# Performance work log

Measured on AMD Instinct MI355X. Metric: run time of the kernel, lower is better.

## Reference

```python
import jax, jax.numpy as jnp
import numpy as np

N = 100_000
E = 1_600_000
F_IN = 128
HEADS = 8
OUT_H = 8   # per-head channels, concat -> 64
N_CLS = 40
K_HOPS = 10  # truncation order of heat-kernel Taylor series
NEG_SLOPE = 0.2
T_INIT = 5.0


def setup_inputs() -> dict:
    key = jax.random.key(0)
    ks = jax.random.split(key, 10)
    x = jax.random.normal(ks[0], (N, F_IN), jnp.float32)
    edge_index = jax.random.randint(ks[1], (2, E), 0, N, jnp.int32)
    t = jnp.full((F_IN,), T_INIT, jnp.float32)  # per-channel learnable diffusion time
    W1 = jax.random.normal(ks[2], (F_IN, HEADS * OUT_H), jnp.float32) / np.sqrt(F_IN).astype(np.float32)
    a_src1 = jax.random.normal(ks[3], (HEADS, OUT_H), jnp.float32) * 0.1
    a_dst1 = jax.random.normal(ks[4], (HEADS, OUT_H), jnp.float32) * 0.1
    b1 = jnp.zeros((HEADS * OUT_H,), jnp.float32)
    W2 = jax.random.normal(ks[5], (HEADS * OUT_H, N_CLS), jnp.float32) / np.sqrt(HEADS * OUT_H).astype(np.float32)
    a_src2 = jax.random.normal(ks[6], (1, N_CLS), jnp.float32) * 0.1
    a_dst2 = jax.random.normal(ks[7], (1, N_CLS), jnp.float32) * 0.1
    b2 = jnp.zeros((N_CLS,), jnp.float32)
    return {"x": x, "edge_index": edge_index, "t": t, "W1": W1, "a_src1": a_src1,
            "a_dst1": a_dst1, "b1": b1, "W2": W2, "a_src2": a_src2, "a_dst2": a_dst2, "b2": b2}


def _add_self_loops(edge_index, n):
    loop = jnp.arange(n, dtype=edge_index.dtype)
    return jnp.concatenate([edge_index, jnp.stack([loop, loop])], axis=1)


def _diffusion(x, src, dst, t, n):
    # heat kernel: exp(-t) * sum_k t^k/k! * A_hat^k x, per-channel t
    deg = jax.ops.segment_sum(jnp.ones_like(src, jnp.float32), dst, num_segments=n)
    dinv = jnp.where(deg > 0, jax.lax.rsqrt(jnp.maximum(deg, 1.0)), 0.0)
    norm = dinv[src] * dinv[dst]  # [E+N]

    def prop(h):
        return jax.ops.segment_sum(norm[:, None] * h[src], dst, num_segments=n)

    coef0 = jnp.exp(-t)  # [F]

    def step(carry, k):
        h, coef, acc = carry
        h = prop(h)
        coef = coef * t / k
        return (h, coef, acc + coef * h), None

    (_, _, out), _ = jax.lax.scan(step, (x, coef0, coef0 * x),
                                  jnp.arange(1, K_HOPS + 1, dtype=jnp.float32))
    return out


def _gat_layer(x, src, dst, W, a_s, a_d, b, heads, out_ch, concat, n):
    h = (x @ W).reshape(n, heads, out_ch)                  # [N,H,C]
    al_s = jnp.einsum('nhc,hc->nh', h, a_s)                # src attn logits
    al_d = jnp.einsum('nhc,hc->nh', h, a_d)
    e = jax.nn.leaky_relu(al_s[src] + al_d[dst], NEG_SLOPE)  # [E+N, H]
    emax = jax.ops.segment_max(e, dst, num_segments=n)       # stable softmax per target node
    ex = jnp.exp(e - emax[dst])
    denom = jax.ops.segment_sum(ex, dst, num_segments=n)
    alpha = ex / jnp.maximum(denom[dst], 1e-16)               # [E+N, H]
    out = jax.ops.segment_sum(alpha[:, :, None] * h[src], dst, num_segments=n)  # [N,H,C]
    out = out.reshape(n, heads * out_ch) if concat else out.mean(axis=1)
    return out + b


def reference(x, edge_index, t, W1, a_src1, a_dst1, b1, W2, a_src2, a_dst2, b2):
    n = x.shape[0]
    ei = _add_self_loops(edge_index, n)
    src, dst = ei[0], ei[1]
    h = _diffusion(x, src, dst, t, n)
    h = _gat_layer(h, src, dst, W1, a_src1, a_dst1, b1, HEADS, OUT_H, True, n)
    h = jax.nn.elu(h)
    h = _gat_layer(h, src, dst, W2, a_src2, a_dst2, b2, 1, N_CLS, False, n)
    return jax.nn.log_softmax(h, axis=1)
```

## Files before the change

kernel.cpp:

```cpp
#include <hip/hip_runtime.h>
#include <hip/hip_bf16.h>


static __device__ __forceinline__ unsigned pack_bf16x2(float a, float b) {
    __hip_bfloat162 p(__float2bfloat16(a), __float2bfloat16(b));
    return *reinterpret_cast<unsigned*>(&p);
}

__global__ void init_node_kernel(int* deg, int n) {
    int i = blockIdx.x * 256 + threadIdx.x;
    if (i < n) deg[i] = 1;
}

__global__ void edge_deg_kernel(const int* __restrict__ dst, int* deg, int* epos, int E) {
    int e = blockIdx.x * 256 + threadIdx.x;
    if (e < E) epos[e] = atomicAdd(&deg[dst[e]], 1);
}

__global__ void alloc_kernel(const int* __restrict__ deg, float* dinv,
                             int* row_off, int* gcount, int n) {
    int i = blockIdx.x * 256 + threadIdx.x;
    if (i >= n) return;
    int dg = deg[i];
    dinv[i] = rsqrtf((float)dg);
    row_off[i] = atomicAdd(gcount, dg);
}

__global__ void scatter_kernel(const int* __restrict__ ei, const int* __restrict__ row_off,
                               const int* __restrict__ epos, const float* __restrict__ dinv,
                               int2* __restrict__ csr_pair, int E, int n) {
    int e = blockIdx.x * 256 + threadIdx.x;
    if (e < E) {
        int s = ei[e], d = ei[E + e];
        csr_pair[row_off[d] + epos[e]] = make_int2(s, __float_as_int(dinv[s] * dinv[d]));
    } else if (e < E + n) {
        int i = e - E;
        float di = dinv[i];
        csr_pair[row_off[i]] = make_int2(i, __float_as_int(di * di));
    }
}

__global__ void coef_kernel(const float* __restrict__ t, float* coefs) {
    int c = threadIdx.x;
    float tc = t[c];
    float v = expf(-tc);
    coefs[c] = v;
    for (int k = 1; k <= 10; ++k) { v *= tc / (float)k; coefs[k * 128 + c] = v; }
}

__global__ void init_diff_a_kernel(const float4* __restrict__ x4, uint2* __restrict__ h0,
                                   int total4) {
    int i = blockIdx.x * 256 + threadIdx.x;
    if (i >= total4) return;
    float4 xv = x4[i];
    h0[i] = make_uint2(pack_bf16x2(xv.x, xv.y), pack_bf16x2(xv.z, xv.w));
}

__global__ void init_diff_b_kernel(const float4* __restrict__ x4, const float* __restrict__ coefs,
                                   uint2* __restrict__ h0, float4* __restrict__ acc4, int total4) {
    int i = blockIdx.x * 256 + threadIdx.x;
    if (i >= total4) return;
    float4 xv = x4[i];
    h0[i] = make_uint2(pack_bf16x2(xv.x, xv.y), pack_bf16x2(xv.z, xv.w));
    const float4 c = *(const float4*)&coefs[(i & 31) * 4];
    acc4[i] = make_float4(c.x * xv.x, c.y * xv.y, c.z * xv.z, c.w * xv.w);
}

static __device__ __forceinline__ float2 gather_row(
    const int* __restrict__ row_off, const int* __restrict__ deg,
    const int2* __restrict__ csr_pair, const unsigned* __restrict__ h,
    int wid, int lane) {
    int off = row_off[wid];
    int cnt = deg[wid];
    float2 a0 = {0.f, 0.f}, a1 = {0.f, 0.f}, a2 = {0.f, 0.f}, a3 = {0.f, 0.f};
    for (int base = 0; base < cnt; base += 64) {
        int nb = min(64, cnt - base);
        int2 p = {0, 0};
        if (lane < nb) p = csr_pair[off + base + lane];
        int tt = 0;
        for (; tt + 7 < nb; tt += 8) {
            int s0 = __builtin_amdgcn_readlane(p.x, tt);
            int s1 = __builtin_amdgcn_readlane(p.x, tt + 1);
            int s2 = __builtin_amdgcn_readlane(p.x, tt + 2);
            int s3 = __builtin_amdgcn_readlane(p.x, tt + 3);
            int s4 = __builtin_amdgcn_readlane(p.x, tt + 4);
            int s5 = __builtin_amdgcn_readlane(p.x, tt + 5);
            int s6 = __builtin_amdgcn_readlane(p.x, tt + 6);
            int s7 = __builtin_amdgcn_readlane(p.x, tt + 7);
            float w0 = __int_as_float(__builtin_amdgcn_readlane(p.y, tt));
            float w1 = __int_as_float(__builtin_amdgcn_readlane(p.y, tt + 1));
            float w2 = __int_as_float(__builtin_amdgcn_readlane(p.y, tt + 2));
            float w3 = __int_as_float(__builtin_amdgcn_readlane(p.y, tt + 3));
            float w4 = __int_as_float(__builtin_amdgcn_readlane(p.y, tt + 4));
            float w5 = __int_as_float(__builtin_amdgcn_readlane(p.y, tt + 5));
            float w6 = __int_as_float(__builtin_amdgcn_readlane(p.y, tt + 6));
            float w7 = __int_as_float(__builtin_amdgcn_readlane(p.y, tt + 7));
            unsigned u0 = h[(size_t)s0 * 64 + lane];
            unsigned u1 = h[(size_t)s1 * 64 + lane];
            unsigned u2 = h[(size_t)s2 * 64 + lane];
            unsigned u3 = h[(size_t)s3 * 64 + lane];
            unsigned u4 = h[(size_t)s4 * 64 + lane];
            unsigned u5 = h[(size_t)s5 * 64 + lane];
            unsigned u6 = h[(size_t)s6 * 64 + lane];
            unsigned u7 = h[(size_t)s7 * 64 + lane];
            a0.x = fmaf(w0, __uint_as_float(u0 << 16), a0.x);
            a0.y = fmaf(w0, __uint_as_float(u0 & 0xffff0000u), a0.y);
            a1.x = fmaf(w1, __uint_as_float(u1 << 16), a1.x);
            a1.y = fmaf(w1, __uint_as_float(u1 & 0xffff0000u), a1.y);
            a2.x = fmaf(w2, __uint_as_float(u2 << 16), a2.x);
            a2.y = fmaf(w2, __uint_as_float(u2 & 0xffff0000u), a2.y);
            a3.x = fmaf(w3, __uint_as_float(u3 << 16), a3.x);
            a3.y = fmaf(w3, __uint_as_float(u3 & 0xffff0000u), a3.y);
            a0.x = fmaf(w4, __uint_as_float(u4 << 16), a0.x);
            a0.y = fmaf(w4, __uint_as_float(u4 & 0xffff0000u), a0.y);
            a1.x = fmaf(w5, __uint_as_float(u5 << 16), a1.x);
            a1.y = fmaf(w5, __uint_as_float(u5 & 0xffff0000u), a1.y);
            a2.x = fmaf(w6, __uint_as_float(u6 << 16), a2.x);
            a2.y = fmaf(w6, __uint_as_float(u6 & 0xffff0000u), a2.y);
            a3.x = fmaf(w7, __uint_as_float(u7 << 16), a3.x);
            a3.y = fmaf(w7, __uint_as_float(u7 & 0xffff0000u), a3.y);
        }
        for (; tt < nb; ++tt) {
            int s = __builtin_amdgcn_readlane(p.x, tt);
            float w = __int_as_float(__builtin_amdgcn_readlane(p.y, tt));
            unsigned u = h[(size_t)s * 64 + lane];
            a0.x = fmaf(w, __uint_as_float(u << 16), a0.x);
            a0.y = fmaf(w, __uint_as_float(u & 0xffff0000u), a0.y);
        }
    }
    float2 s;
    s.x = (a0.x + a1.x) + (a2.x + a3.x);
    s.y = (a0.y + a1.y) + (a2.y + a3.y);
    return s;
}

__global__ void hop_a_kernel(const int* __restrict__ row_off, const int* __restrict__ deg,
                             const int2* __restrict__ csr_pair,
                             const unsigned* __restrict__ h_prev, unsigned* __restrict__ h_out,
                             int n) {
    int wid = (blockIdx.x << 2) + (threadIdx.x >> 6);
    int lane = threadIdx.x & 63;
    if (wid >= n) return;
    float2 s = gather_row(row_off, deg, csr_pair, h_prev, wid, lane);
    h_out[(size_t)wid * 64 + lane] = pack_bf16x2(s.x, s.y);
}

__global__ void hop_b_kernel(const int* __restrict__ row_off, const int* __restrict__ deg,
                             const int2* __restrict__ csr_pair,
                             const unsigned* __restrict__ h_prev, unsigned* __restrict__ h_out,
                             float2* __restrict__ acc2, const float2* __restrict__ coefk2,
                             int n, int write_h) {
    int wid = (blockIdx.x << 2) + (threadIdx.x >> 6);
    int lane = threadIdx.x & 63;
    if (wid >= n) return;
    float2 s = gather_row(row_off, deg, csr_pair, h_prev, wid, lane);
    size_t o = (size_t)wid * 64 + lane;
    if (write_h) h_out[o] = pack_bf16x2(s.x, s.y);
    float2 c = coefk2[lane];
    float2 av = acc2[o];
    av.x = fmaf(c.x, s.x, av.x);
    av.y = fmaf(c.y, s.y, av.y);
    acc2[o] = av;
}

__global__ void combine_kernel(const float2* __restrict__ x2, const float* __restrict__ coefs,
                               const unsigned* __restrict__ hseq, size_t stride,
                               float2* __restrict__ acc2, int total) {
    int i = blockIdx.x * 256 + threadIdx.x;
    if (i >= total) return;
    int c2 = i & 63;
    const float2* coefs2 = (const float2*)coefs;
    float2 c0 = coefs2[c2];
    float2 xv = x2[i];
    float2 a = make_float2(c0.x * xv.x, c0.y * xv.y);
#pragma unroll
    for (int k = 1; k <= 10; ++k) {
        float2 ck = coefs2[(size_t)k * 64 + c2];
        unsigned u = hseq[(size_t)k * stride + i];
        a.x = fmaf(ck.x, __uint_as_float(u << 16), a.x);
        a.y = fmaf(ck.y, __uint_as_float(u & 0xffff0000u), a.y);
    }
    acc2[i] = a;
}

__global__ __launch_bounds__(256) void gemm1_kernel(
    const float* __restrict__ acc, const float* __restrict__ W1,
    const float* __restrict__ a_s, const float* __restrict__ a_d,
    unsigned* __restrict__ h1b, float* __restrict__ als, float* __restrict__ ald, int n) {
    __shared__ float Wl[128 * 64];
    __shared__ float Al[4][16 * 128];
    for (int i = threadIdx.x; i < 128 * 64; i += 256) Wl[i] = W1[i];
    int w = threadIdx.x >> 6;
    int lane = threadIdx.x & 63;
    int node0 = (blockIdx.x * 4 + w) * 16;
    const float4* accv4 = (const float4*)acc;
    float4* Av4 = (float4*)Al[w];
#pragma unroll
    for (int i = 0; i < 8; ++i) {
        int f4 = i * 64 + lane;
        int g4 = node0 * 32 + f4;
        float4 v = (g4 < n * 32) ? accv4[g4] : make_float4(0.f, 0.f, 0.f, 0.f);
        Av4[f4] = v;
    }
    __syncthreads();
    float sums[16];
#pragma unroll
    for (int nd = 0; nd < 16; ++nd) sums[nd] = 0.f;
#pragma unroll 1
    for (int kc = 0; kc < 16; ++kc) {
        float wr[8];
#pragma unroll
        for (int i = 0; i < 8; ++i) wr[i] = Wl[(kc * 8 + i) * 64 + lane];
#pragma unroll
        for (int nd = 0; nd < 16; ++nd) {
            float4 a = *(const float4*)&Al[w][nd * 128 + kc * 8];
            float4 b = *(const float4*)&Al[w][nd * 128 + kc * 8 + 4];
            float s = sums[nd];
            s = fmaf(wr[0], a.x, s); s = fmaf(wr[1], a.y, s);
            s = fmaf(wr[2], a.z, s); s = fmaf(wr[3], a.w, s);
            s = fmaf(wr[4], b.x, s); s = fmaf(wr[5], b.y, s);
            s = fmaf(wr[6], b.z, s); s = fmaf(wr[7], b.w, s);
            sums[nd] = s;
        }
    }
    float asv = a_s[lane], adv = a_d[lane];
#pragma unroll
    for (int nd = 0; nd < 16; ++nd) {
        int node = node0 + nd;
        if (node >= n) break;
        float sum = sums[nd];
        float partner = __shfl_xor(sum, 1);
        if ((lane & 1) == 0) h1b[(size_t)node * 32 + (lane >> 1)] = pack_bf16x2(sum, partner);
        float vs = sum * asv;
        float vd = sum * adv;
        vs += __shfl_xor(vs, 1); vs += __shfl_xor(vs, 2); vs += __shfl_xor(vs, 4);
        vd += __shfl_xor(vd, 1); vd += __shfl_xor(vd, 2); vd += __shfl_xor(vd, 4);
        if ((lane & 7) == 0) {
            als[(size_t)node * 8 + (lane >> 3)] = vs;
            ald[(size_t)node * 8 + (lane >> 3)] = vd;
        }
    }
}

__global__ void agg1_kernel(const int* __restrict__ row_off, const int* __restrict__ deg,
                            const int2* __restrict__ csr_pair,
                            const unsigned* __restrict__ h1b, const float* __restrict__ als,
                            const float* __restrict__ ald, const float* __restrict__ b1,
                            float2* __restrict__ helu2, int n) {
    int wid = (blockIdx.x << 2) + (threadIdx.x >> 6);
    int lane = threadIdx.x & 63;
    if (wid >= n) return;
    int half = lane >> 5;
    int l = lane & 31;
    int head = l >> 2;
    int off = row_off[wid];
    int cnt = deg[wid];
    float aldv = ald[(size_t)wid * 8 + head];
    float dA = 0.f, dB = 0.f;
    float2 aA = {0.f, 0.f}, aB = {0.f, 0.f};
    for (int base = 0; base < cnt; base += 64) {
        int nb = min(64, cnt - base);
        int srcv = 0;
        if (lane < nb) srcv = csr_pair[off + base + lane].x;
        int j = 0;
        for (; j + 3 < nb; j += 4) {
            int sA0 = __builtin_amdgcn_readlane(srcv, j);
            int sA1 = __builtin_amdgcn_readlane(srcv, j + 1);
            int sB0 = __builtin_amdgcn_readlane(srcv, j + 2);
            int sB1 = __builtin_amdgcn_readlane(srcv, j + 3);
            int sA = half ? sA1 : sA0;
            int sB = half ? sB1 : sB0;
            float eA = als[(size_t)sA * 8 + head] + aldv;
            float eB = als[(size_t)sB * 8 + head] + aldv;
            eA = eA > 0.f ? eA : 0.2f * eA;
            eB = eB > 0.f ? eB : 0.2f * eB;
            float pA = __expf(eA);
            float pB = __expf(eB);
            unsigned uA = h1b[(size_t)sA * 32 + l];
            unsigned uB = h1b[(size_t)sB * 32 + l];
            dA += pA; dB += pB;
            aA.x = fmaf(pA, __uint_as_float(uA << 16), aA.x);
            aA.y = fmaf(pA, __uint_as_float(uA & 0xffff0000u), aA.y);
            aB.x = fmaf(pB, __uint_as_float(uB << 16), aB.x);
            aB.y = fmaf(pB, __uint_as_float(uB & 0xffff0000u), aB.y);
        }
        for (; j < nb; j += 2) {
            int s0 = __builtin_amdgcn_readlane(srcv, j);
            int s1 = (j + 1 < nb) ? __builtin_amdgcn_readlane(srcv, j + 1) : -1;
            int s = half ? s1 : s0;
            bool valid = s >= 0;
            int ss = valid ? s : 0;
            float e = als[(size_t)ss * 8 + head] + aldv;
            e = e > 0.f ? e : 0.2f * e;
            float p = valid ? __expf(e) : 0.f;
            unsigned u = h1b[(size_t)ss * 32 + l];
            dA += p;
            aA.x = fmaf(p, __uint_as_float(u << 16), aA.x);
            aA.y = fmaf(p, __uint_as_float(u & 0xffff0000u), aA.y);
        }
    }
    float d = dA + dB;
    float2 accv = make_float2(aA.x + aB.x, aA.y + aB.y);
    d += __shfl_xor(d, 32);
    accv.x += __shfl_xor(accv.x, 32);
    accv.y += __shfl_xor(accv.y, 32);
    if (half == 0) {
        float inv = 1.f / d;
        float ox = fmaf(accv.x, inv, b1[2 * l]);
        float oy = fmaf(accv.y, inv, b1[2 * l + 1]);
        ox = ox > 0.f ? ox : expm1f(ox);
        oy = oy > 0.f ? oy : expm1f(oy);
        helu2[(size_t)wid * 32 + l] = make_float2(ox, oy);
    }
}

__global__ __launch_bounds__(256) void gemm2_kernel(
    const float* __restrict__ helu, const float* __restrict__ W2,
    const float* __restrict__ a_s, const float* __restrict__ a_d,
    unsigned* __restrict__ h2b, float* __restrict__ als, float* __restrict__ ald, int n) {
    __shared__ float Wl[64 * 40];
    __shared__ float Al[4][16 * 64];
    for (int i = threadIdx.x; i < 64 * 40; i += 256) Wl[i] = W2[i];
    int w = threadIdx.x >> 6;
    int lane = threadIdx.x & 63;
    int node0 = (blockIdx.x * 4 + w) * 16;
    const float4* hv4 = (const float4*)helu;
    float4* Av4 = (float4*)Al[w];
#pragma unroll
    for (int i = 0; i < 4; ++i) {
        int f4 = i * 64 + lane;
        int g4 = node0 * 16 + f4;
        float4 v = (g4 < n * 16) ? hv4[g4] : make_float4(0.f, 0.f, 0.f, 0.f);
        Av4[f4] = v;
    }
    __syncthreads();
    bool act = lane < 40;
    int li = act ? lane : 0;
    float sums[16];
#pragma unroll
    for (int nd = 0; nd < 16; ++nd) sums[nd] = 0.f;
#pragma unroll 1
    for (int kc = 0; kc < 8; ++kc) {
        float wr[8];
#pragma unroll
        for (int i = 0; i < 8; ++i) wr[i] = Wl[(kc * 8 + i) * 40 + li];
#pragma unroll
        for (int nd = 0; nd < 16; ++nd) {
            float4 a = *(const float4*)&Al[w][nd * 64 + kc * 8];
            float4 b = *(const float4*)&Al[w][nd * 64 + kc * 8 + 4];
            float s = sums[nd];
            s = fmaf(wr[0], a.x, s); s = fmaf(wr[1], a.y, s);
            s = fmaf(wr[2], a.z, s); s = fmaf(wr[3], a.w, s);
            s = fmaf(wr[4], b.x, s); s = fmaf(wr[5], b.y, s);
            s = fmaf(wr[6], b.z, s); s = fmaf(wr[7], b.w, s);
            sums[nd] = s;
        }
    }
    float asv = act ? a_s[lane] : 0.f;
    float adv = act ? a_d[lane] : 0.f;
#pragma unroll
    for (int nd = 0; nd < 16; ++nd) {
        int node = node0 + nd;
        if (node >= n) break;
        float sum = sums[nd];
        float partner = __shfl_xor(sum, 1);
        if (act && (lane & 1) == 0) h2b[(size_t)node * 20 + (lane >> 1)] = pack_bf16x2(sum, partner);
        float vs = act ? sum * asv : 0.f;
        float vd = act ? sum * adv : 0.f;
#pragma unroll
        for (int i = 32; i >= 1; i >>= 1) { vs += __shfl_xor(vs, i); vd += __shfl_xor(vd, i); }
        if (lane == 0) { als[node] = vs; ald[node] = vd; }
    }
}

__global__ void agg2_kernel(const int* __restrict__ row_off, const int* __restrict__ deg,
                            const int2* __restrict__ csr_pair,
                            const unsigned* __restrict__ h2b, const float* __restrict__ als,
                            const float* __restrict__ ald, const float* __restrict__ b2,
                            float* __restrict__ out, int n) {
    int wid = (blockIdx.x << 2) + (threadIdx.x >> 6);
    int lane = threadIdx.x & 63;
    if (wid >= n) return;
    int half = lane >> 5;
    int l = lane & 31;
    bool act = l < 20;
    int li = act ? l : 0;
    int off = row_off[wid];
    int cnt = deg[wid];
    float aldv = ald[wid];
    float dA = 0.f, dB = 0.f;
    float2 aA = {0.f, 0.f}, aB = {0.f, 0.f};
    for (int base = 0; base < cnt; base += 64) {
        int nb = min(64, cnt - base);
        int srcv = 0;
        if (lane < nb) srcv = csr_pair[off + base + lane].x;
        int j = 0;
        for (; j + 3 < nb; j += 4) {
            int sA0 = __builtin_amdgcn_readlane(srcv, j);
            int sA1 = __builtin_amdgcn_readlane(srcv, j + 1);
            int sB0 = __builtin_amdgcn_readlane(srcv, j + 2);
            int sB1 = __builtin_amdgcn_readlane(srcv, j + 3);
            int sA = half ? sA1 : sA0;
            int sB = half ? sB1 : sB0;
            float eA = als[sA] + aldv;
            float eB = als[sB] + aldv;
            eA = eA > 0.f ? eA : 0.2f * eA;
            eB = eB > 0.f ? eB : 0.2f * eB;
            float pA = __expf(eA);
            float pB = __expf(eB);
            unsigned uA = h2b[(size_t)sA * 20 + li];
            unsigned uB = h2b[(size_t)sB * 20 + li];
            dA += pA; dB += pB;
            aA.x = fmaf(pA, __uint_as_float(uA << 16), aA.x);
            aA.y = fmaf(pA, __uint_as_float(uA & 0xffff0000u), aA.y);
            aB.x = fmaf(pB, __uint_as_float(uB << 16), aB.x);
            aB.y = fmaf(pB, __uint_as_float(uB & 0xffff0000u), aB.y);
        }
        for (; j < nb; j += 2) {
            int s0 = __builtin_amdgcn_readlane(srcv, j);
            int s1 = (j + 1 < nb) ? __builtin_amdgcn_readlane(srcv, j + 1) : -1;
            int s = half ? s1 : s0;
            bool valid = s >= 0;
            int ss = valid ? s : 0;
            float e = als[ss] + aldv;
            e = e > 0.f ? e : 0.2f * e;
            float p = valid ? __expf(e) : 0.f;
            unsigned u = h2b[(size_t)ss * 20 + li];
            dA += p;
            aA.x = fmaf(p, __uint_as_float(u << 16), aA.x);
            aA.y = fmaf(p, __uint_as_float(u & 0xffff0000u), aA.y);
        }
    }
    float d = dA + dB;
    float2 accv = make_float2(aA.x + aB.x, aA.y + aB.y);
    d += __shfl_xor(d, 32);
    accv.x += __shfl_xor(accv.x, 32);
    accv.y += __shfl_xor(accv.y, 32);
    float inv = 1.f / d;
    bool live = (half == 0) && act;
    float ox = live ? fmaf(accv.x, inv, b2[2 * l]) : -1e30f;
    float oy = live ? fmaf(accv.y, inv, b2[2 * l + 1]) : -1e30f;
    float vv = fmaxf(ox, oy);
#pragma unroll
    for (int i = 16; i >= 1; i >>= 1) vv = fmaxf(vv, __shfl_xor(vv, i));
    float ex = live ? (__expf(ox - vv) + __expf(oy - vv)) : 0.f;
#pragma unroll
    for (int i = 16; i >= 1; i >>= 1) ex += __shfl_xor(ex, i);
    if (live) {
        float lse = vv + logf(ex);
        *(float2*)&out[(size_t)wid * 40 + 2 * l] = make_float2(ox - lse, oy - lse);
    }
}

extern "C" void kernel_launch(void* const* d_in, const int* in_sizes, int n_in,
                              void* d_out, int out_size, void* d_ws, size_t ws_size,
                              hipStream_t stream) {
    const float* x    = (const float*)d_in[0];
    const int*   ei   = (const int*)d_in[1];
    const float* t    = (const float*)d_in[2];
    const float* W1   = (const float*)d_in[3];
    const float* a_s1 = (const float*)d_in[4];
    const float* a_d1 = (const float*)d_in[5];
    const float* b1   = (const float*)d_in[6];
    const float* W2   = (const float*)d_in[7];
    const float* a_s2 = (const float*)d_in[8];
    const float* a_d2 = (const float*)d_in[9];
    const float* b2   = (const float*)d_in[10];
    float* out = (float*)d_out;

    const int N = in_sizes[0] / 128;
    const int E = in_sizes[1] / 2;

    char* w = (char*)d_ws;
    auto carve = [&](size_t bytes) {
        void* p = (void*)w;
        w += (bytes + 255) & ~(size_t)255;
        return p;
    };
    int*      deg      = (int*)carve((size_t)N * 4);
    int*      row_off  = (int*)carve((size_t)N * 4);
    int*      gcount   = (int*)carve(256);
    float*    dinv     = (float*)carve((size_t)N * 4);
    int*      epos     = (int*)carve((size_t)E * 4);
    int2*     csr_pair = (int2*)carve((size_t)(E + N) * 8);
    float*    coefs    = (float*)carve(11 * 128 * 4);
    float*    als1     = (float*)carve((size_t)N * 8 * 4);
    float*    ald1     = (float*)carve((size_t)N * 8 * 4);
    float*    als2     = (float*)carve((size_t)N * 4);
    float*    ald2     = (float*)carve((size_t)N * 4);
    float*    acc      = (float*)carve((size_t)N * 128 * 4);
    unsigned* h1b      = (unsigned*)carve((size_t)N * 32 * 4);
    float*    helu     = (float*)carve((size_t)N * 64 * 4);
    unsigned* h2b      = (unsigned*)carve((size_t)N * 20 * 4);

    size_t szh = (size_t)N * 64 * 4;
    size_t used = (size_t)(w - (char*)d_ws);
    size_t remain = (ws_size > used) ? ws_size - used : 0;
    bool pathA = remain >= 11 * szh;
    unsigned* hseq = (unsigned*)w;
    size_t strideU = (size_t)N * 64;

    dim3 blk(256);
    int gN = (N + 255) / 256;
    int gE = (E + 255) / 256;
    int gEN = (E + N + 255) / 256;
    int gW = (N + 3) / 4;
    int gT = (N + 63) / 64;

    init_node_kernel<<<gN, blk, 0, stream>>>(deg, N);
    hipMemsetAsync(gcount, 0, 4, stream);
    edge_deg_kernel<<<gE, blk, 0, stream>>>(ei + E, deg, epos, E);
    alloc_kernel<<<gN, blk, 0, stream>>>(deg, dinv, row_off, gcount, N);
    scatter_kernel<<<gEN, blk, 0, stream>>>(ei, row_off, epos, dinv, csr_pair, E, N);
    coef_kernel<<<1, 128, 0, stream>>>(t, coefs);

    if (pathA) {
        init_diff_a_kernel<<<(N * 32 + 255) / 256, blk, 0, stream>>>(
            (const float4*)x, (uint2*)hseq, N * 32);
        for (int k = 1; k <= 10; ++k) {
            hop_a_kernel<<<gW, blk, 0, stream>>>(row_off, deg, csr_pair,
                                                 hseq + (size_t)(k - 1) * strideU,
                                                 hseq + (size_t)k * strideU, N);
        }
        combine_kernel<<<(N * 64 + 255) / 256, blk, 0, stream>>>(
            (const float2*)x, coefs, hseq, strideU, (float2*)acc, N * 64);
    } else {
        unsigned* hA = hseq;
        unsigned* hB = hseq + strideU;
        init_diff_b_kernel<<<(N * 32 + 255) / 256, blk, 0, stream>>>(
            (const float4*)x, coefs, (uint2*)hA, (float4*)acc, N * 32);
        unsigned* hc = hA;
        unsigned* hn = hB;
        for (int k = 1; k <= 10; ++k) {
            hop_b_kernel<<<gW, blk, 0, stream>>>(row_off, deg, csr_pair, hc, hn, (float2*)acc,
                                                 (const float2*)(coefs + k * 128), N,
                                                 k < 10 ? 1 : 0);
            unsigned* tmp = hc; hc = hn; hn = tmp;
        }
    }

    gemm1_kernel<<<gT, blk, 0, stream>>>(acc, W1, a_s1, a_d1, h1b, als1, ald1, N);
    agg1_kernel<<<gW, blk, 0, stream>>>(row_off, deg, csr_pair, h1b, als1, ald1, b1,
                                        (float2*)helu, N);
    gemm2_kernel<<<gT, blk, 0, stream>>>(helu, W2, a_s2, a_d2, h2b, als2, ald2, N);
    agg2_kernel<<<gW, blk, 0, stream>>>(row_off, deg, csr_pair, h2b, als2, ald2, b2, out, N);
}
```

Before: 1.274 ms.

## Ping-pong diffusion buffers with paired accumulation and bf16 LDS in gemm1

Replaces the path that stored all ten hop results in separate buffers and combined them at the end. The diffusion now ping-pongs between two bf16 buffers and folds every two hops into the fp32 accumulator with a small elementwise kernel. This keeps the working set of the propagation small enough to stay cache-resident, at the cost of extra read-modify-write passes over the accumulator. gemm1 also stages W1 and the accumulator tile in LDS as bf16, halving LDS use to raise occupancy, which adds rounding error to the first GEMM input.

```diff
diff --git a/kernel.cpp b/kernel.cpp
--- a/kernel.cpp
+++ b/kernel.cpp
@@ -5,6 +5,12 @@
 static __device__ __forceinline__ unsigned pack_bf16x2(float a, float b) {
     __hip_bfloat162 p(__float2bfloat16(a), __float2bfloat16(b));
     return *reinterpret_cast<unsigned*>(&p);
+}
+static __device__ __forceinline__ float bf16lo(unsigned u) {
+    return __uint_as_float(u << 16);
+}
+static __device__ __forceinline__ float bf16hi(unsigned u) {
+    return __uint_as_float(u & 0xffff0000u);
 }
 
 __global__ void init_node_kernel(int* deg, int n) {
@@ -48,22 +54,12 @@
     for (int k = 1; k <= 10; ++k) { v *= tc / (float)k; coefs[k * 128 + c] = v; }
 }
 
-__global__ void init_diff_a_kernel(const float4* __restrict__ x4, uint2* __restrict__ h0,
-                                   int total4) {
+__global__ void init_diff_kernel(const float4* __restrict__ x4, uint2* __restrict__ h0,
+                                 int total4) {
     int i = blockIdx.x * 256 + threadIdx.x;
     if (i >= total4) return;
     float4 xv = x4[i];
     h0[i] = make_uint2(pack_bf16x2(xv.x, xv.y), pack_bf16x2(xv.z, xv.w));
-}
-
-__global__ void init_diff_b_kernel(const float4* __restrict__ x4, const float* __restrict__ coefs,
-                                   uint2* __restrict__ h0, float4* __restrict__ acc4, int total4) {
-    int i = blockIdx.x * 256 + threadIdx.x;
-    if (i >= total4) return;
-    float4 xv = x4[i];
-    h0[i] = make_uint2(pack_bf16x2(xv.x, xv.y), pack_bf16x2(xv.z, xv.w));
-    const float4 c = *(const float4*)&coefs[(i & 31) * 4];
-    acc4[i] = make_float4(c.x * xv.x, c.y * xv.y, c.z * xv.z, c.w * xv.w);
 }
 
 static __device__ __forceinline__ float2 gather_row(
@@ -103,29 +99,20 @@
             unsigned u5 = h[(size_t)s5 * 64 + lane];
             unsigned u6 = h[(size_t)s6 * 64 + lane];
             unsigned u7 = h[(size_t)s7 * 64 + lane];
-            a0.x = fmaf(w0, __uint_as_float(u0 << 16), a0.x);
-            a0.y = fmaf(w0, __uint_as_float(u0 & 0xffff0000u), a0.y);
-            a1.x = fmaf(w1, __uint_as_float(u1 << 16), a1.x);
-            a1.y = fmaf(w1, __uint_as_float(u1 & 0xffff0000u), a1.y);
-            a2.x = fmaf(w2, __uint_as_float(u2 << 16), a2.x);
-            a2.y = fmaf(w2, __uint_as_float(u2 & 0xffff0000u), a2.y);
-            a3.x = fmaf(w3, __uint_as_float(u3 << 16), a3.x);
-            a3.y = fmaf(w3, __uint_as_float(u3 & 0xffff0000u), a3.y);
-            a0.x = fmaf(w4, __uint_as_float(u4 << 16), a0.x);
-            a0.y = fmaf(w4, __uint_as_float(u4 & 0xffff0000u), a0.y);
-            a1.x = fmaf(w5, __uint_as_float(u5 << 16), a1.x);
-            a1.y = fmaf(w5, __uint_as_float(u5 & 0xffff0000u), a1.y);
-            a2.x = fmaf(w6, __uint_as_float(u6 << 16), a2.x);
-            a2.y = fmaf(w6, __uint_as_float(u6 & 0xffff0000u), a2.y);
-            a3.x = fmaf(w7, __uint_as_float(u7 << 16), a3.x);
-            a3.y = fmaf(w7, __uint_as_float(u7 & 0xffff0000u), a3.y);
+            a0.x = fmaf(w0, bf16lo(u0), a0.x); a0.y = fmaf(w0, bf16hi(u0), a0.y);
+            a1.x = fmaf(w1, bf16lo(u1), a1.x); a1.y = fmaf(w1, bf16hi(u1), a1.y);
+            a2.x = fmaf(w2, bf16lo(u2), a2.x); a2.y = fmaf(w2, bf16hi(u2), a2.y);
+            a3.x = fmaf(w3, bf16lo(u3), a3.x); a3.y = fmaf(w3, bf16hi(u3), a3.y);
+            a0.x = fmaf(w4, bf16lo(u4), a0.x); a0.y = fmaf(w4, bf16hi(u4), a0.y);
+            a1.x = fmaf(w5, bf16lo(u5), a1.x); a1.y = fmaf(w5, bf16hi(u5), a1.y);
+            a2.x = fmaf(w6, bf16lo(u6), a2.x); a2.y = fmaf(w6, bf16hi(u6), a2.y);
+            a3.x = fmaf(w7, bf16lo(u7), a3.x); a3.y = fmaf(w7, bf16hi(u7), a3.y);
         }
         for (; tt < nb; ++tt) {
             int s = __builtin_amdgcn_readlane(p.x, tt);
             float w = __int_as_float(__builtin_amdgcn_readlane(p.y, tt));
             unsigned u = h[(size_t)s * 64 + lane];
-            a0.x = fmaf(w, __uint_as_float(u << 16), a0.x);
-            a0.y = fmaf(w, __uint_as_float(u & 0xffff0000u), a0.y);
+            a0.x = fmaf(w, bf16lo(u), a0.x); a0.y = fmaf(w, bf16hi(u), a0.y);
         }
     }
     float2 s;
@@ -134,10 +121,10 @@
     return s;
 }
 
-__global__ void hop_a_kernel(const int* __restrict__ row_off, const int* __restrict__ deg,
-                             const int2* __restrict__ csr_pair,
-                             const unsigned* __restrict__ h_prev, unsigned* __restrict__ h_out,
-                             int n) {
+__global__ void hop_kernel(const int* __restrict__ row_off, const int* __restrict__ deg,
+                           const int2* __restrict__ csr_pair,
+                           const unsigned* __restrict__ h_prev, unsigned* __restrict__ h_out,
+                           int n) {
     int wid = (blockIdx.x << 2) + (threadIdx.x >> 6);
     int lane = threadIdx.x & 63;
     if (wid >= n) return;
@@ -145,62 +132,62 @@
     h_out[(size_t)wid * 64 + lane] = pack_bf16x2(s.x, s.y);
 }
 
-__global__ void hop_b_kernel(const int* __restrict__ row_off, const int* __restrict__ deg,
-                             const int2* __restrict__ csr_pair,
-                             const unsigned* __restrict__ h_prev, unsigned* __restrict__ h_out,
-                             float2* __restrict__ acc2, const float2* __restrict__ coefk2,
-                             int n, int write_h) {
-    int wid = (blockIdx.x << 2) + (threadIdx.x >> 6);
-    int lane = threadIdx.x & 63;
-    if (wid >= n) return;
-    float2 s = gather_row(row_off, deg, csr_pair, h_prev, wid, lane);
-    size_t o = (size_t)wid * 64 + lane;
-    if (write_h) h_out[o] = pack_bf16x2(s.x, s.y);
-    float2 c = coefk2[lane];
-    float2 av = acc2[o];
-    av.x = fmaf(c.x, s.x, av.x);
-    av.y = fmaf(c.y, s.y, av.y);
-    acc2[o] = av;
-}
-
-__global__ void combine_kernel(const float2* __restrict__ x2, const float* __restrict__ coefs,
-                               const unsigned* __restrict__ hseq, size_t stride,
-                               float2* __restrict__ acc2, int total) {
+__global__ void acc_first_kernel(const float4* __restrict__ x4,
+                                 const uint2* __restrict__ hA, const uint2* __restrict__ hB,
+                                 const float* __restrict__ coefs,
+                                 float4* __restrict__ acc4, int total4) {
     int i = blockIdx.x * 256 + threadIdx.x;
-    if (i >= total) return;
-    int c2 = i & 63;
-    const float2* coefs2 = (const float2*)coefs;
-    float2 c0 = coefs2[c2];
-    float2 xv = x2[i];
-    float2 a = make_float2(c0.x * xv.x, c0.y * xv.y);
-#pragma unroll
-    for (int k = 1; k <= 10; ++k) {
-        float2 ck = coefs2[(size_t)k * 64 + c2];
-        unsigned u = hseq[(size_t)k * stride + i];
-        a.x = fmaf(ck.x, __uint_as_float(u << 16), a.x);
-        a.y = fmaf(ck.y, __uint_as_float(u & 0xffff0000u), a.y);
-    }
-    acc2[i] = a;
+    if (i >= total4) return;
+    int c4 = (i & 31) * 4;
+    const float4 c0 = *(const float4*)&coefs[c4];
+    const float4 cA = *(const float4*)&coefs[128 + c4];
+    const float4 cB = *(const float4*)&coefs[256 + c4];
+    float4 xv = x4[i];
+    uint2 ua = hA[i];
+    uint2 ub = hB[i];
+    float4 a;
+    a.x = c0.x * xv.x + cA.x * bf16lo(ua.x) + cB.x * bf16lo(ub.x);
+    a.y = c0.y * xv.y + cA.y * bf16hi(ua.x) + cB.y * bf16hi(ub.x);
+    a.z = c0.z * xv.z + cA.z * bf16lo(ua.y) + cB.z * bf16lo(ub.y);
+    a.w = c0.w * xv.w + cA.w * bf16hi(ua.y) + cB.w * bf16hi(ub.y);
+    acc4[i] = a;
+}
+
+__global__ void acc_pair_kernel(const uint2* __restrict__ hA, const uint2* __restrict__ hB,
+                                const float* __restrict__ coefA, const float* __restrict__ coefB,
+                                float4* __restrict__ acc4, int total4) {
+    int i = blockIdx.x * 256 + threadIdx.x;
+    if (i >= total4) return;
+    int c4 = (i & 31) * 4;
+    const float4 cA = *(const float4*)&coefA[c4];
+    const float4 cB = *(const float4*)&coefB[c4];
+    uint2 ua = hA[i];
+    uint2 ub = hB[i];
+    float4 a = acc4[i];
+    a.x += cA.x * bf16lo(ua.x) + cB.x * bf16lo(ub.x);
+    a.y += cA.y * bf16hi(ua.x) + cB.y * bf16hi(ub.x);
+    a.z += cA.z * bf16lo(ua.y) + cB.z * bf16lo(ub.y);
+    a.w += cA.w * bf16hi(ua.y) + cB.w * bf16hi(ub.y);
+    acc4[i] = a;
 }
 
 __global__ __launch_bounds__(256) void gemm1_kernel(
     const float* __restrict__ acc, const float* __restrict__ W1,
     const float* __restrict__ a_s, const float* __restrict__ a_d,
     unsigned* __restrict__ h1b, float* __restrict__ als, float* __restrict__ ald, int n) {
-    __shared__ float Wl[128 * 64];
-    __shared__ float Al[4][16 * 128];
-    for (int i = threadIdx.x; i < 128 * 64; i += 256) Wl[i] = W1[i];
+    __shared__ unsigned short Wl16[128 * 64];
+    __shared__ unsigned Al[4][16 * 64];
+    for (int i = threadIdx.x; i < 128 * 64; i += 256)
+        Wl16[i] = (unsigned short)(pack_bf16x2(W1[i], 0.f) & 0xffffu);
     int w = threadIdx.x >> 6;
     int lane = threadIdx.x & 63;
     int node0 = (blockIdx.x * 4 + w) * 16;
-    const float4* accv4 = (const float4*)acc;
-    float4* Av4 = (float4*)Al[w];
-#pragma unroll
-    for (int i = 0; i < 8; ++i) {
-        int f4 = i * 64 + lane;
-        int g4 = node0 * 32 + f4;
-        float4 v = (g4 < n * 32) ? accv4[g4] : make_float4(0.f, 0.f, 0.f, 0.f);
-        Av4[f4] = v;
+    const float2* acc2 = (const float2*)acc;
+#pragma unroll
+    for (int i = 0; i < 16; ++i) {
+        int node = node0 + i;
+        float2 v = (node < n) ? acc2[(size_t)node * 64 + lane] : make_float2(0.f, 0.f);
+        Al[w][i * 64 + lane] = pack_bf16x2(v.x, v.y);
     }
     __syncthreads();
     float sums[16];
@@ -210,16 +197,16 @@
     for (int kc = 0; kc < 16; ++kc) {
         float wr[8];
 #pragma unroll
-        for (int i = 0; i < 8; ++i) wr[i] = Wl[(kc * 8 + i) * 64 + lane];
+        for (int i = 0; i < 8; ++i)
+            wr[i] = __uint_as_float((unsigned)Wl16[(kc * 8 + i) * 64 + lane] << 16);
 #pragma unroll
         for (int nd = 0; nd < 16; ++nd) {
-            float4 a = *(const float4*)&Al[w][nd * 128 + kc * 8];
-            float4 b = *(const float4*)&Al[w][nd * 128 + kc * 8 + 4];
+            uint4 u = *(const uint4*)&Al[w][nd * 64 + kc * 4];
             float s = sums[nd];
-            s = fmaf(wr[0], a.x, s); s = fmaf(wr[1], a.y, s);
-            s = fmaf(wr[2], a.z, s); s = fmaf(wr[3], a.w, s);
-            s = fmaf(wr[4], b.x, s); s = fmaf(wr[5], b.y, s);
-            s = fmaf(wr[6], b.z, s); s = fmaf(wr[7], b.w, s);
+            s = fmaf(wr[0], bf16lo(u.x), s); s = fmaf(wr[1], bf16hi(u.x), s);
+            s = fmaf(wr[2], bf16lo(u.y), s); s = fmaf(wr[3], bf16hi(u.y), s);
+            s = fmaf(wr[4], bf16lo(u.z), s); s = fmaf(wr[5], bf16hi(u.z), s);
+            s = fmaf(wr[6], bf16lo(u.w), s); s = fmaf(wr[7], bf16hi(u.w), s);
             sums[nd] = s;
         }
     }
@@ -279,10 +266,10 @@
             unsigned uA = h1b[(size_t)sA * 32 + l];
             unsigned uB = h1b[(size_t)sB * 32 + l];
             dA += pA; dB += pB;
-            aA.x = fmaf(pA, __uint_as_float(uA << 16), aA.x);
-            aA.y = fmaf(pA, __uint_as_float(uA & 0xffff0000u), aA.y);
-            aB.x = fmaf(pB, __uint_as_float(uB << 16), aB.x);
-            aB.y = fmaf(pB, __uint_as_float(uB & 0xffff0000u), aB.y);
+            aA.x = fmaf(pA, bf16lo(uA), aA.x);
+            aA.y = fmaf(pA, bf16hi(uA), aA.y);
+            aB.x = fmaf(pB, bf16lo(uB), aB.x);
+            aB.y = fmaf(pB, bf16hi(uB), aB.y);
         }
         for (; j < nb; j += 2) {
             int s0 = __builtin_amdgcn_readlane(srcv, j);
@@ -295,8 +282,8 @@
             float p = valid ? __expf(e) : 0.f;
             unsigned u = h1b[(size_t)ss * 32 + l];
             dA += p;
-            aA.x = fmaf(p, __uint_as_float(u << 16), aA.x);
-            aA.y = fmaf(p, __uint_as_float(u & 0xffff0000u), aA.y);
+            aA.x = fmaf(p, bf16lo(u), aA.x);
+            aA.y = fmaf(p, bf16hi(u), aA.y);
         }
     }
     float d = dA + dB;
@@ -411,10 +398,10 @@
             unsigned uA = h2b[(size_t)sA * 20 + li];
             unsigned uB = h2b[(size_t)sB * 20 + li];
             dA += pA; dB += pB;
-            aA.x = fmaf(pA, __uint_as_float(uA << 16), aA.x);
-            aA.y = fmaf(pA, __uint_as_float(uA & 0xffff0000u), aA.y);
-            aB.x = fmaf(pB, __uint_as_float(uB << 16), aB.x);
-            aB.y = fmaf(pB, __uint_as_float(uB & 0xffff0000u), aB.y);
+            aA.x = fmaf(pA, bf16lo(uA), aA.x);
+            aA.y = fmaf(pA, bf16hi(uA), aA.y);
+            aB.x = fmaf(pB, bf16lo(uB), aB.x);
+            aB.y = fmaf(pB, bf16hi(uB), aB.y);
         }
         for (; j < nb; j += 2) {
             int s0 = __builtin_amdgcn_readlane(srcv, j);
@@ -427,8 +414,8 @@
             float p = valid ? __expf(e) : 0.f;
             unsigned u = h2b[(size_t)ss * 20 + li];
             dA += p;
-            aA.x = fmaf(p, __uint_as_float(u << 16), aA.x);
-            aA.y = fmaf(p, __uint_as_float(u & 0xffff0000u), aA.y);
+            aA.x = fmaf(p, bf16lo(u), aA.x);
+            aA.y = fmaf(p, bf16hi(u), aA.y);
         }
     }
     float d = dA + dB;
@@ -489,16 +476,11 @@
     float*    als2     = (float*)carve((size_t)N * 4);
     float*    ald2     = (float*)carve((size_t)N * 4);
     float*    acc      = (float*)carve((size_t)N * 128 * 4);
+    unsigned* hA       = (unsigned*)carve((size_t)N * 64 * 4);
+    unsigned* hB       = (unsigned*)carve((size_t)N * 64 * 4);
     unsigned* h1b      = (unsigned*)carve((size_t)N * 32 * 4);
     float*    helu     = (float*)carve((size_t)N * 64 * 4);
     unsigned* h2b      = (unsigned*)carve((size_t)N * 20 * 4);
-
-    size_t szh = (size_t)N * 64 * 4;
-    size_t used = (size_t)(w - (char*)d_ws);
-    size_t remain = (ws_size > used) ? ws_size - used : 0;
-    bool pathA = remain >= 11 * szh;
-    unsigned* hseq = (unsigned*)w;
-    size_t strideU = (size_t)N * 64;
 
     dim3 blk(256);
     int gN = (N + 255) / 256;
@@ -506,6 +488,7 @@
     int gEN = (E + N + 255) / 256;
     int gW = (N + 3) / 4;
     int gT = (N + 63) / 64;
+    int gS = (N * 32 + 255) / 256;
 
     init_node_kernel<<<gN, blk, 0, stream>>>(deg, N);
     hipMemsetAsync(gcount, 0, 4, stream);
@@ -513,29 +496,22 @@
     alloc_kernel<<<gN, blk, 0, stream>>>(deg, dinv, row_off, gcount, N);
     scatter_kernel<<<gEN, blk, 0, stream>>>(ei, row_off, epos, dinv, csr_pair, E, N);
     coef_kernel<<<1, 128, 0, stream>>>(t, coefs);
-
-    if (pathA) {
-        init_diff_a_kernel<<<(N * 32 + 255) / 256, blk, 0, stream>>>(
-            (const float4*)x, (uint2*)hseq, N * 32);
-        for (int k = 1; k <= 10; ++k) {
-            hop_a_kernel<<<gW, blk, 0, stream>>>(row_off, deg, csr_pair,
-                                                 hseq + (size_t)(k - 1) * strideU,
-                                                 hseq + (size_t)k * strideU, N);
-        }
-        combine_kernel<<<(N * 64 + 255) / 256, blk, 0, stream>>>(
-            (const float2*)x, coefs, hseq, strideU, (float2*)acc, N * 64);
-    } else {
-        unsigned* hA = hseq;
-        unsigned* hB = hseq + strideU;
-        init_diff_b_kernel<<<(N * 32 + 255) / 256, blk, 0, stream>>>(
-            (const float4*)x, coefs, (uint2*)hA, (float4*)acc, N * 32);
-        unsigned* hc = hA;
-        unsigned* hn = hB;
-        for (int k = 1; k <= 10; ++k) {
-            hop_b_kernel<<<gW, blk, 0, stream>>>(row_off, deg, csr_pair, hc, hn, (float2*)acc,
-                                                 (const float2*)(coefs + k * 128), N,
-                                                 k < 10 ? 1 : 0);
-            unsigned* tmp = hc; hc = hn; hn = tmp;
+    init_diff_kernel<<<gS, blk, 0, stream>>>((const float4*)x, (uint2*)hA, N * 32);
+
+    unsigned* hc = hA;
+    unsigned* hn = hB;
+    for (int k = 1; k <= 10; ++k) {
+        hop_kernel<<<gW, blk, 0, stream>>>(row_off, deg, csr_pair, hc, hn, N);
+        unsigned* tmp = hc; hc = hn; hn = tmp;
+        if (k == 2) {
+            acc_first_kernel<<<gS, blk, 0, stream>>>(
+                (const float4*)x, (const uint2*)hB, (const uint2*)hA, coefs,
+                (float4*)acc, N * 32);
+        } else if ((k & 1) == 0) {
+            acc_pair_kernel<<<gS, blk, 0, stream>>>(
+                (const uint2*)hB, (const uint2*)hA,
+                coefs + (size_t)(k - 1) * 128, coefs + (size_t)k * 128,
+                (float4*)acc, N * 32);
         }
     }
 
```

New measurement: 1.259 ms. No clear change (-1.2%).
